# Kernel optimization log

Measured on AMD Instinct MI355X. Metric: run time of the kernel, lower is better.

Reference implementation:

```python
import jax, jax.numpy as jnp
import numpy as np

NUM_LAYERS = 3
INPUT_SIZE = 32
NUM_CAT = 64
EMB = 64
NQ = 1            # num_queries
B = 16
N = 2048
DIN = INPUT_SIZE + NUM_CAT + EMB  # 160, columns of W_e_proj


def setup_inputs() -> dict:
    key = jax.random.key(0)
    k1, k2, k3, k4 = jax.random.split(key, 4)
    return {
        "x": jax.random.normal(k1, (B, DIN, N), dtype=jnp.float32),
        "alpha": jax.random.normal(k2, (NUM_LAYERS, EMB), dtype=jnp.float32),
        "kernel_param": jnp.ones((1,), dtype=jnp.float32),
        "embedding_matrix": jax.random.normal(k3, (EMB, NUM_CAT), dtype=jnp.float32),
        "M": jax.random.normal(k4, (EMB, EMB), dtype=jnp.float32),
    }


def reference(x, alpha, kernel_param, embedding_matrix, M):
    # Input projection h = W_e_proj @ x. W_e_proj is block-structured:
    #   rows [0,is)        : identity on x[:is]
    #   rows [is, is+emb)  : embedding_matrix @ x[is:is+num_cat]
    #   rows [-emb:]       : identity on x[-emb:]
    h = jnp.concatenate([
        x[:, :INPUT_SIZE],
        jnp.einsum('ec,bcn->ben', embedding_matrix,
                   x[:, INPUT_SIZE:INPUT_SIZE + NUM_CAT]),
        x[:, -EMB:],
    ], axis=1)  # [B, INPUT_SIZE + 2*EMB, N]

    kp = kernel_param[0]
    for nl in range(NUM_LAYERS):
        kv = h[:, :, :-NQ]          # keys/values exclude the query tokens
        n_ctx = kv.shape[-1]
        # W_Q, W_K are identity on the first INPUT_SIZE rows, zero elsewhere
        xq = h[:, :INPUT_SIZE]      # [B, is, N]
        xk = kv[:, :INPUT_SIZE]     # [B, is, Nk]
        # linear kernel scores
        scores = kp * jnp.einsum('bim,bin->bmn', xq, xk)   # [B, N, Nk]
        # W_V is zero except diag(alpha[nl]) on the middle EMB block
        v_mid = alpha[nl][:, None] * kv[:, INPUT_SIZE:INPUT_SIZE + EMB]  # [B, EMB, Nk]
        attn_mid = jnp.einsum('bin,bmn->bim', v_mid, scores) / n_ctx     # [B, EMB, N]
        # Output projection P^T: middle rows get M @ attn_mid,
        # bottom EMB rows get attn_mid (identity), first rows zero.
        upd = jnp.concatenate([
            jnp.zeros((h.shape[0], INPUT_SIZE, h.shape[2]), h.dtype),
            jnp.einsum('ji,bim->bjm', M, attn_mid),
            attn_mid,
        ], axis=1)
        h = h + upd

    f = h[:, -EMB:, :]                                    # [B, EMB, N]
    logits = jnp.einsum('bdn,dc->bnc', f, embedding_matrix)  # [B, N, C]
    predictions = jax.nn.softmax(logits, axis=-1)
    return logits, predictions
```

## Files before the change

kernel.cpp:

```cpp
#include <hip/hip_runtime.h>

#define BB 16
#define NN 2048
#define DIN 160
#define IS 32
#define NCAT 64
#define EMBD 64
#define NCTX 2047

__global__ __launch_bounds__(256) void k_gram(const float* __restrict__ x,
                                              float* __restrict__ Pg,
                                              float* __restrict__ Pk) {
    __shared__ float xs[128][100];
    const int t = threadIdx.x;
    const int blk = blockIdx.x;
    const int b = blk >> 4;
    const int tile = blk & 15;
    const int n0 = tile << 7;
    const float* xb = x + (size_t)b * DIN * NN;

    for (int idx = t; idx < 96 * 32; idx += 256) {
        const int r = idx >> 5;
        const int m4 = (idx & 31) << 2;
        float4 v = *(const float4*)&xb[r * NN + n0 + m4];
        xs[m4 + 0][r] = v.x; xs[m4 + 1][r] = v.y;
        xs[m4 + 2][r] = v.z; xs[m4 + 3][r] = v.w;
    }
    __syncthreads();

    const int nlim = (tile == 15) ? 127 : 128;
    const int i = t >> 3;
    const int d0 = (t & 7) << 2;
    float4 g = {0,0,0,0}, k0 = {0,0,0,0}, k1 = {0,0,0,0};
    for (int m = 0; m < nlim; m++) {
        float4 q = *(const float4*)&xs[m][d0];
        const float a  = xs[m][i];
        const float c0 = xs[m][32 + i];
        const float c1 = xs[m][64 + i];
        g.x  += a  * q.x; g.y  += a  * q.y; g.z  += a  * q.z; g.w  += a  * q.w;
        k0.x += c0 * q.x; k0.y += c0 * q.y; k0.z += c0 * q.z; k0.w += c0 * q.w;
        k1.x += c1 * q.x; k1.y += c1 * q.y; k1.z += c1 * q.z; k1.w += c1 * q.w;
    }
    *(float4*)&Pg[(size_t)blk * 1024 + i * 32 + d0] = g;
    float* pk = Pk + (size_t)blk * 2048;
    *(float4*)&pk[i * 32 + d0] = k0;
    *(float4*)&pk[(i + 32) * 32 + d0] = k1;
}

__global__ __launch_bounds__(256) void k_chain(const float* __restrict__ Pg,
                                               const float* __restrict__ Pk,
                                               const float* __restrict__ alpha,
                                               const float* __restrict__ kp,
                                               const float* __restrict__ emb,
                                               const float* __restrict__ Mm,
                                               float* __restrict__ Ubuf) {
    __shared__ float G_s[32][36];
    __shared__ float K_s[64][36];
    __shared__ float C_s[64][36];
    __shared__ float W_s[64][36];
    __shared__ float T_s[64][36];
    const int t = threadIdx.x;
    const int b = blockIdx.x;

    for (int idx = t; idx < 1024; idx += 256) {
        float s = 0.f;
#pragma unroll
        for (int g = 0; g < 16; g++) s += Pg[((size_t)(b * 16 + g)) * 1024 + idx];
        G_s[idx >> 5][idx & 31] = s;
    }
    for (int idx = t; idx < 2048; idx += 256) {
        float s = 0.f;
#pragma unroll
        for (int g = 0; g < 16; g++) s += Pk[((size_t)(b * 16 + g)) * 2048 + idx];
        K_s[idx >> 5][idx & 31] = s;
    }
    __syncthreads();

    const int r  = t >> 2;
    const int dd = (t & 3) << 3;

    {
        const float* er = emb + r * EMBD;
        float acc[8];
#pragma unroll
        for (int j = 0; j < 8; j++) acc[j] = 0.f;
        for (int c = 0; c < 64; c++) {
            const float e = er[c];
#pragma unroll
            for (int j = 0; j < 8; j++) acc[j] += e * K_s[c][dd + j];
        }
#pragma unroll
        for (int j = 0; j < 8; j++) C_s[r][dd + j] = acc[j];
    }
    __syncthreads();

    const float scale = kp[0] * (1.f / (float)NCTX);
    for (int l = 0; l < 3; l++) {
        const float f = scale * alpha[l * EMBD + r];
#pragma unroll
        for (int j = 0; j < 8; j++) {
            const float w = f * C_s[r][dd + j];
            if (l == 0) W_s[r][dd + j] = w; else W_s[r][dd + j] += w;
        }
        if (l < 2) {
            float crow[32];
#pragma unroll
            for (int d = 0; d < 32; d++) crow[d] = C_s[r][d];
            float tacc[8];
#pragma unroll
            for (int j = 0; j < 8; j++) tacc[j] = 0.f;
            for (int d = 0; d < 32; d++) {
                const float cv = crow[d];
#pragma unroll
                for (int j = 0; j < 8; j++) tacc[j] += cv * G_s[d][dd + j];
            }
#pragma unroll
            for (int j = 0; j < 8; j++) T_s[r][dd + j] = f * tacc[j];
            __syncthreads();
            const float* Mr = Mm + r * EMBD;
            float uacc[8];
#pragma unroll
            for (int j = 0; j < 8; j++) uacc[j] = 0.f;
            for (int jj = 0; jj < 64; jj++) {
                const float mv = Mr[jj];
#pragma unroll
                for (int j = 0; j < 8; j++) uacc[j] += mv * T_s[jj][dd + j];
            }
#pragma unroll
            for (int j = 0; j < 8; j++) C_s[r][dd + j] += uacc[j];
            __syncthreads();
        }
    }
    __syncthreads();

    {
        float acc[8];
#pragma unroll
        for (int j = 0; j < 8; j++) acc[j] = 0.f;
        for (int e = 0; e < 64; e++) {
            const float ev = emb[e * EMBD + r];
#pragma unroll
            for (int j = 0; j < 8; j++) acc[j] += ev * W_s[e][dd + j];
        }
        float* Ur = Ubuf + (size_t)b * 2048 + r * 32 + dd;
#pragma unroll
        for (int j = 0; j < 8; j++) Ur[j] = acc[j];
    }
}

__global__ __launch_bounds__(256) void k_out(const float* __restrict__ x,
                                             const float* __restrict__ emb,
                                             const float* __restrict__ Ubuf,
                                             float* __restrict__ out) {
    __shared__ float lg_s[128][68];
    const int t = threadIdx.x;
    const int blk = blockIdx.x;
    const int b = blk >> 4;
    const int tile = blk & 15;
    const int h = t >> 7;
    const int nl = t & 127;
    const int n = (tile << 7) + nl;
    const int c0 = h << 5;
    const float* xb = x + (size_t)b * DIN * NN;

    float xq[IS];
#pragma unroll
    for (int d = 0; d < IS; d++) xq[d] = xb[d * NN + n];

    float lg[32];
    const float* Ub = Ubuf + (size_t)b * 2048;
#pragma unroll 4
    for (int cl = 0; cl < 32; cl++) {
        const float* Ur = Ub + (c0 + cl) * 32;
        float s = 0.f;
#pragma unroll
        for (int k = 0; k < 8; k++) {
            float4 u = *(const float4*)&Ur[4 * k];
            s += u.x * xq[4*k] + u.y * xq[4*k+1] + u.z * xq[4*k+2] + u.w * xq[4*k+3];
        }
        lg[cl] = s;
    }
    for (int e = 0; e < 64; e++) {
        const float tv = xb[(IS + NCAT + e) * NN + n];
        const float* er = emb + e * EMBD + c0;
#pragma unroll
        for (int cl = 0; cl < 32; cl++) lg[cl] += er[cl] * tv;
    }

    const size_t base = ((size_t)b * NN + n) * (size_t)NCAT;
    float* lo = out + base + c0;
#pragma unroll
    for (int k = 0; k < 8; k++) {
        float4 v = {lg[4*k], lg[4*k+1], lg[4*k+2], lg[4*k+3]};
        *(float4*)&lo[4*k] = v;
        *(float4*)&lg_s[nl][c0 + 4*k] = v;
    }
    __syncthreads();

    const int o0 = (1 - h) << 5;
    float mx = lg[0];
#pragma unroll
    for (int cl = 1; cl < 32; cl++) mx = fmaxf(mx, lg[cl]);
    float og[32];
#pragma unroll
    for (int k = 0; k < 8; k++) {
        float4 v = *(const float4*)&lg_s[nl][o0 + 4*k];
        og[4*k] = v.x; og[4*k+1] = v.y; og[4*k+2] = v.z; og[4*k+3] = v.w;
    }
#pragma unroll
    for (int cl = 0; cl < 32; cl++) mx = fmaxf(mx, og[cl]);

    float sum = 0.f;
#pragma unroll
    for (int cl = 0; cl < 32; cl++) {
        lg[cl] = __expf(lg[cl] - mx);
        sum += lg[cl];
    }
#pragma unroll
    for (int cl = 0; cl < 32; cl++) sum += __expf(og[cl] - mx);

    const float inv = 1.f / sum;
    float* po = out + (size_t)BB * NN * NCAT + base + c0;
#pragma unroll
    for (int k = 0; k < 8; k++) {
        float4 v = {lg[4*k]*inv, lg[4*k+1]*inv, lg[4*k+2]*inv, lg[4*k+3]*inv};
        *(float4*)&po[4*k] = v;
    }
}

extern "C" void kernel_launch(void* const* d_in, const int* in_sizes, int n_in,
                              void* d_out, int out_size, void* d_ws, size_t ws_size,
                              hipStream_t stream) {
    const float* x     = (const float*)d_in[0];
    const float* alpha = (const float*)d_in[1];
    const float* kp    = (const float*)d_in[2];
    const float* emb   = (const float*)d_in[3];
    const float* Mmat  = (const float*)d_in[4];
    float* out = (float*)d_out;

    float* Pg   = (float*)d_ws;
    float* Pk   = Pg + (size_t)256 * 1024;
    float* Ubuf = Pk + (size_t)256 * 2048;

    k_gram <<<256, 256, 0, stream>>>(x, Pg, Pk);
    k_chain<<<16,  256, 0, stream>>>(Pg, Pk, alpha, kp, emb, Mmat, Ubuf);
    k_out  <<<256, 256, 0, stream>>>(x, emb, Ubuf, out);
}
```

Before: 140.0 us.

## Fuse gram and chain kernels via last-block atomic counter per batch

Merges the gram-partial kernel and the per-batch chain kernel into one launch. The 16 tile blocks of each batch increment an atomic counter, and the last one to finish reduces the partials and runs the chain. This removes one kernel launch and its dependency gap, at the cost of an extra memset, threadfences, and more shared memory per block, which may reduce occupancy of the gram phase. It also unrolls the gram loop by two and drops a register copy of the C row.

After: 172.0 us. +22.8%, slower.

```diff
diff --git a/kernel.cpp b/kernel.cpp
--- a/kernel.cpp
+++ b/kernel.cpp
@@ -8,9 +8,13 @@
 #define EMBD 64
 #define NCTX 2047
 
-__global__ __launch_bounds__(256) void k_gram(const float* __restrict__ x,
-                                              float* __restrict__ Pg,
-                                              float* __restrict__ Pk) {
+__global__ __launch_bounds__(256) void k_gram_chain(
+    const float* __restrict__ x, const float* __restrict__ alpha,
+    const float* __restrict__ kp, const float* __restrict__ emb,
+    const float* __restrict__ Mm,
+    float* __restrict__ Pg, float* __restrict__ Pk,
+    float* __restrict__ Ubuf, int* __restrict__ cnt)
+{
     __shared__ float xs[128][100];
     const int t = threadIdx.x;
     const int blk = blockIdx.x;
@@ -32,6 +36,7 @@
     const int i = t >> 3;
     const int d0 = (t & 7) << 2;
     float4 g = {0,0,0,0}, k0 = {0,0,0,0}, k1 = {0,0,0,0};
+#pragma unroll 2
     for (int m = 0; m < nlim; m++) {
         float4 q = *(const float4*)&xs[m][d0];
         const float a  = xs[m][i];
@@ -45,33 +50,31 @@
     float* pk = Pk + (size_t)blk * 2048;
     *(float4*)&pk[i * 32 + d0] = k0;
     *(float4*)&pk[(i + 32) * 32 + d0] = k1;
-}
-
-__global__ __launch_bounds__(256) void k_chain(const float* __restrict__ Pg,
-                                               const float* __restrict__ Pk,
-                                               const float* __restrict__ alpha,
-                                               const float* __restrict__ kp,
-                                               const float* __restrict__ emb,
-                                               const float* __restrict__ Mm,
-                                               float* __restrict__ Ubuf) {
+
+    __shared__ int lastflag;
+    __threadfence();
+    __syncthreads();
+    if (t == 0) lastflag = (atomicAdd(&cnt[b], 1) == 15);
+    __syncthreads();
+    if (!lastflag) return;
+    __threadfence();
+
     __shared__ float G_s[32][36];
     __shared__ float K_s[64][36];
     __shared__ float C_s[64][36];
     __shared__ float W_s[64][36];
     __shared__ float T_s[64][36];
-    const int t = threadIdx.x;
-    const int b = blockIdx.x;
 
     for (int idx = t; idx < 1024; idx += 256) {
         float s = 0.f;
 #pragma unroll
-        for (int g = 0; g < 16; g++) s += Pg[((size_t)(b * 16 + g)) * 1024 + idx];
+        for (int gg = 0; gg < 16; gg++) s += Pg[((size_t)(b * 16 + gg)) * 1024 + idx];
         G_s[idx >> 5][idx & 31] = s;
     }
     for (int idx = t; idx < 2048; idx += 256) {
         float s = 0.f;
 #pragma unroll
-        for (int g = 0; g < 16; g++) s += Pk[((size_t)(b * 16 + g)) * 2048 + idx];
+        for (int gg = 0; gg < 16; gg++) s += Pk[((size_t)(b * 16 + gg)) * 2048 + idx];
         K_s[idx >> 5][idx & 31] = s;
     }
     __syncthreads();
@@ -103,14 +106,11 @@
             if (l == 0) W_s[r][dd + j] = w; else W_s[r][dd + j] += w;
         }
         if (l < 2) {
-            float crow[32];
-#pragma unroll
-            for (int d = 0; d < 32; d++) crow[d] = C_s[r][d];
             float tacc[8];
 #pragma unroll
             for (int j = 0; j < 8; j++) tacc[j] = 0.f;
             for (int d = 0; d < 32; d++) {
-                const float cv = crow[d];
+                const float cv = C_s[r][d];
 #pragma unroll
                 for (int j = 0; j < 8; j++) tacc[j] += cv * G_s[d][dd + j];
             }
@@ -241,8 +241,9 @@
     float* Pg   = (float*)d_ws;
     float* Pk   = Pg + (size_t)256 * 1024;
     float* Ubuf = Pk + (size_t)256 * 2048;
-
-    k_gram <<<256, 256, 0, stream>>>(x, Pg, Pk);
-    k_chain<<<16,  256, 0, stream>>>(Pg, Pk, alpha, kp, emb, Mmat, Ubuf);
-    k_out  <<<256, 256, 0, stream>>>(x, emb, Ubuf, out);
+    int*   cnt  = (int*)(Ubuf + (size_t)16 * 2048);
+
+    hipMemsetAsync(cnt, 0, BB * sizeof(int), stream);
+    k_gram_chain<<<256, 256, 0, stream>>>(x, alpha, kp, emb, Mmat, Pg, Pk, Ubuf, cnt);
+    k_out<<<256, 256, 0, stream>>>(x, emb, Ubuf, out);
 }
```
